# Kernel optimization log

Hardware: AMD Instinct MI355X
Metric: run time of the kernel (lower is better)

The kernel has to match this reference:

```python
import jax, jax.numpy as jnp
import numpy as np

NUM_PROJS = 7
BLOCK = 32

def _gray_perm(n):
    # unit-hamming-distance (Gray-code) permutation used by AngularLSH
    a = np.array([0, 1], dtype=np.int32)
    for s in range(2, n + 1):
        a = np.concatenate([a, a[::-1] + 2 ** (s - 1)])
    return a

PERM = jnp.asarray(_gray_perm(NUM_PROJS))
ENC = jnp.asarray(2 ** np.arange(NUM_PROJS), dtype=np.int32)  # [R]


def lsh_hash(x, proj_dir):
    # x: [B,H,S,D], proj_dir: [D,R] -> integer bucket ids [B,H,S]
    bits = (jnp.einsum('bhsd,dr->bhsr', x, proj_dir) > 0).astype(jnp.int32)
    code = (bits * ENC).sum(-1)
    return PERM[code]


def sdpa(q, k, v, mask):
    # q,k,v: [...,S,D]; mask: bool broadcastable to [...,Sq,Sk]
    scale = q.shape[-1] ** -0.5
    scores = jnp.einsum('...qd,...kd->...qk', q, k) * scale
    scores = jnp.where(mask, scores, -jnp.inf)
    return jnp.einsum('...qk,...kd->...qd', jax.nn.softmax(scores, axis=-1), v)


def setup_inputs() -> dict:
    key = jax.random.key(0)
    kq, kk, kv, kp = jax.random.split(key, 4)
    B, H, S, D = 2, 16, 2048, 128
    return {
        'q': jax.random.normal(kq, (B, H, S, D), dtype=jnp.float32),
        'k': jax.random.normal(kk, (B, H, S, D), dtype=jnp.float32),
        'v': jax.random.normal(kv, (B, H, S, D), dtype=jnp.float32),
        'proj_dir': jax.random.normal(kp, (D, NUM_PROJS), dtype=jnp.float32),
        'mask': jnp.ones((1, 1, 1, 1), dtype=bool),
    }


def reference(q, k, v, proj_dir, mask):
    B, H, S, D = q.shape
    # 1) LSH hash queries, stable sort along seq dim, reorder queries
    q_hash = lsh_hash(q, proj_dir)                                   # [B,H,S]
    sort_idx = jnp.argsort(q_hash, axis=2, stable=True)              # [B,H,S]
    q_hash_sorted = jnp.take_along_axis(q_hash, sort_idx, axis=2)
    q_sorted = jnp.take_along_axis(q, sort_idx[..., None], axis=2)   # [B,H,S,D]
    # 2) hash keys (unsorted), split into blocks of size BLOCK
    k_hash = lsh_hash(k, proj_dir)                                   # [B,H,S]
    k_hash_blk = k_hash.reshape(-1, 1, BLOCK)                        # [NB,1,32]
    q_hash_blk = q_hash_sorted.reshape(-1, 1, BLOCK)
    # 3) criticality: per-block count of matching hash ids; critical blocks get K zeroed
    criticality = (k_hash_blk == q_hash_blk).sum(-1).squeeze(-1)     # [NB]
    keep = (criticality <= 0).astype(q.dtype)                        # 0 where critical (matches torch loop)
    Qb = q_sorted.reshape(-1, 1, BLOCK, D)                           # [NB,1,32,D]
    Kb = k.reshape(-1, 1, BLOCK, D) * keep[:, None, None, None]
    Vb = v.reshape(-1, 1, BLOCK, D)
    # 4) dual SDPA: blocked critical attention + full dense attention
    out_critical = sdpa(Qb, Kb, Vb, mask).reshape(B, H, S, D)
    out_actual = sdpa(q, k, v, mask)                                 # [B,H,S,D]
    loss = jnp.mean((out_critical - out_actual) ** 2)
    return out_actual, loss
```

## Files before the change

kernel.cpp:

```cpp
#include <hip/hip_runtime.h>
#include <hip/hip_bf16.h>

#define SEQ 2048
#define DIM 128
#define NBH 32
#define NROWS (NBH*SEQ)
#define NBLK (NROWS/32)
#define SCALE 0.08838834764831845f
#define QSC (0.08838834764831845f * 1.4426950408889634f)

typedef __attribute__((ext_vector_type(8))) short short8;
typedef __attribute__((ext_vector_type(16))) float float16;

__device__ __forceinline__ unsigned short f2bf(float x) {
    union { float f; unsigned u; } v; v.f = x;
    unsigned r = v.u + 0x7fffu + ((v.u >> 16) & 1u);
    return (unsigned short)(r >> 16);
}
__device__ __forceinline__ unsigned pack_bf16(float a, float b) {
    float2 f; f.x = a; f.y = b;
    __hip_bfloat162 h = __float22bfloat162_rn(f);
    union { __hip_bfloat162 h2; unsigned u; } cv; cv.h2 = h; return cv.u;
}
__device__ __forceinline__ void gl_lds16(const void* g, void* l) {
    __builtin_amdgcn_global_load_lds((const __attribute__((address_space(1))) unsigned int*)g,
                                     (__attribute__((address_space(3))) unsigned int*)l, 16, 0, 0);
}

__global__ __launch_bounds__(256) void hash_kernel(const float* __restrict__ qg, const float* __restrict__ kg,
                            const float* __restrict__ proj,
                            int* __restrict__ qh, int* __restrict__ kh)
{
    const int gw   = (int)((blockIdx.x * blockDim.x + threadIdx.x) >> 6);
    const int lane = threadIdx.x & 63;
    const int sub  = lane >> 4;
    const int dl   = (lane & 15) * 8;
    const int r    = gw * 4 + sub;
    const float* src; int* dst; int row;
    if (r < NROWS) { src = qg; dst = qh; row = r; }
    else           { src = kg; dst = kh; row = r - NROWS; }

    const float* x = src + (size_t)row * DIM + dl;
    float xv[8];
    {
        float4 f0 = *(const float4*)x;
        float4 f1 = *(const float4*)(x + 4);
        xv[0]=f0.x; xv[1]=f0.y; xv[2]=f0.z; xv[3]=f0.w;
        xv[4]=f1.x; xv[5]=f1.y; xv[6]=f1.z; xv[7]=f1.w;
    }
    float pj[56];
    #pragma unroll
    for (int i = 0; i < 14; ++i)
        *(float4*)&pj[i*4] = *(const float4*)(proj + dl*7 + i*4);

    float a[7] = {0.f,0.f,0.f,0.f,0.f,0.f,0.f};
    #pragma unroll
    for (int d = 0; d < 8; ++d)
        #pragma unroll
        for (int p = 0; p < 7; ++p) a[p] = fmaf(xv[d], pj[d*7+p], a[p]);

    #pragma unroll
    for (int off = 1; off < 16; off <<= 1)
        #pragma unroll
        for (int p = 0; p < 7; ++p) a[p] += __shfl_xor(a[p], off, 64);

    if ((lane & 15) == 0) {
        int code = 0;
        if (a[0] > 0.f) code |= 1;  if (a[1] > 0.f) code |= 2;
        if (a[2] > 0.f) code |= 4;  if (a[3] > 0.f) code |= 8;
        if (a[4] > 0.f) code |= 16; if (a[5] > 0.f) code |= 32;
        if (a[6] > 0.f) code |= 64;
        dst[row] = code ^ (code >> 1);
    }
}

__global__ __launch_bounds__(256) void sort_kernel(const int* __restrict__ qh,
                                                   int* __restrict__ sidx, int* __restrict__ qhs)
{
    __shared__ unsigned short cnt[128][260];
    __shared__ int startv[128];
    const int bh = blockIdx.x;
    const int t  = threadIdx.x;
    const int base = bh*SEQ;

    for (int i = t; i < 128*260; i += 256) ((unsigned short*)cnt)[i] = 0;
    __syncthreads();

    int hv[8];
    {
        int4 a = *(const int4*)(qh + base + t*8);
        int4 b = *(const int4*)(qh + base + t*8 + 4);
        hv[0]=a.x; hv[1]=a.y; hv[2]=a.z; hv[3]=a.w;
        hv[4]=b.x; hv[5]=b.y; hv[6]=b.z; hv[7]=b.w;
    }
    #pragma unroll
    for (int i = 0; i < 8; ++i) cnt[hv[i]][t]++;
    __syncthreads();

    const int wv = t >> 6, l = t & 63;
    #pragma unroll 1
    for (int v = wv; v < 128; v += 4) {
        ushort4 cc = *(const ushort4*)&cnt[v][4*l];
        unsigned c0 = cc.x, c1 = cc.y, c2 = cc.z, c3 = cc.w;
        unsigned s01 = c0 + c1;
        unsigned s = s01 + c2 + c3;
        unsigned inc = s;
        #pragma unroll
        for (int off = 1; off < 64; off <<= 1) {
            unsigned o = __shfl_up(inc, off, 64);
            if (l >= off) inc += o;
        }
        unsigned ex = inc - s;
        ushort4 wb;
        wb.x = (unsigned short)ex;
        wb.y = (unsigned short)(ex + c0);
        wb.z = (unsigned short)(ex + s01);
        wb.w = (unsigned short)(ex + s01 + c2);
        *(ushort4*)&cnt[v][4*l] = wb;
        if (l == 63) cnt[v][256] = (unsigned short)inc;
    }
    __syncthreads();

    if (t < 64) {
        int a0 = cnt[2*t][256], a1 = cnt[2*t+1][256];
        int s2 = a0 + a1, inc = s2;
        #pragma unroll
        for (int off = 1; off < 64; off <<= 1) {
            int o = __shfl_up(inc, off, 64);
            if (t >= off) inc += o;
        }
        int ex = inc - s2;
        startv[2*t]   = ex;
        startv[2*t+1] = ex + a0;
    }
    __syncthreads();

    #pragma unroll
    for (int i = 0; i < 8; ++i) {
        const int v = hv[i];
        int prior = 0;
        #pragma unroll
        for (int j = 0; j < 8; ++j) if (j < i && hv[j] == v) ++prior;
        const int rank = startv[v] + (int)cnt[v][t] + prior;
        sidx[base + rank] = t*8 + i;
        qhs[base + rank]  = v;
    }
}

__global__ __launch_bounds__(256) void prep_kernel(const float* __restrict__ kg,
                                                   const float* __restrict__ vg,
                                                   unsigned short* __restrict__ kbf,
                                                   unsigned short* __restrict__ vtg)
{
    __shared__ unsigned short T[128][72];
    const int t  = threadIdx.x;
    const int h  = blockIdx.x >> 5;
    const int sl = blockIdx.x & 31;
    const size_t base = ((size_t)h*SEQ + sl*64) * DIM;

    #pragma unroll
    for (int i = 0; i < 8; ++i) {
        const float4 f = *(const float4*)(kg + base + ((size_t)i*256 + t)*4);
        uint2 pk; pk.x = pack_bf16(f.x, f.y); pk.y = pack_bf16(f.z, f.w);
        *(uint2*)(kbf + base + ((size_t)i*256 + t)*4) = pk;
    }

    const int kk = t & 63, seg = t >> 6;
    #pragma unroll
    for (int i = 0; i < 8; ++i) {
        float4 f = *(const float4*)(vg + base + (size_t)kk*DIM + seg*32 + i*4);
        T[seg*32 + i*4 + 0][kk] = f2bf(f.x);
        T[seg*32 + i*4 + 1][kk] = f2bf(f.y);
        T[seg*32 + i*4 + 2][kk] = f2bf(f.z);
        T[seg*32 + i*4 + 3][kk] = f2bf(f.w);
    }
    __syncthreads();
    const int r = t >> 1, hf = t & 1;
    unsigned short* dst = vtg + ((size_t)h*DIM + r)*SEQ + sl*64 + hf*32;
    #pragma unroll
    for (int i = 0; i < 4; ++i)
        *(short8*)(dst + i*8) = *(const short8*)&T[r][hf*32 + i*8];
}

__global__ __launch_bounds__(256, 2) void dense_attn_mfma(
    const unsigned short* __restrict__ kbf, const unsigned short* __restrict__ vtg,
    const float* __restrict__ qg, float* __restrict__ outg)
{
    __shared__ __align__(16) unsigned short KbF[2*8192];
    __shared__ __align__(16) unsigned short VbF[2*8192];

    const int t    = threadIdx.x;
    const int lane = t & 63;
    const int w    = t >> 6;
    const int q5   = lane >> 5;
    const int l31  = lane & 31;
    const int lvec = lane * 8;

    const int b    = blockIdx.x;
    const int slot = b >> 3;
    const int head = (b & 7) * 4 + (slot >> 4);
    const int qblk = slot & 15;

    const float* Qg = qg + ((size_t)head*SEQ + qblk*128 + w*32) * DIM;
    const unsigned short* Kh = kbf + (size_t)head*SEQ*DIM;
    const unsigned short* Vh = vtg + (size_t)head*DIM*SEQ;

    const unsigned short* kgp[4]; unsigned short* kls[4];
    const unsigned short* vgp[4]; unsigned short* vls[4];
    {
        const int ks = w >> 1, vs = w >> 1, vc = w & 1;
        #pragma unroll
        for (int i = 0; i < 4; ++i) {
            const int kch = (w & 1) * 4 + i;
            kgp[i] = Kh + (size_t)(ks*32 + l31)*DIM + kch*16 + q5*8;
            kls[i] = KbF + (ks*8 + kch)*512;
            vgp[i] = Vh + (size_t)(i*32 + l31)*SEQ + vs*32 + vc*16 + q5*8;
            vls[i] = VbF + (vs*8 + vc*4 + i)*512;
        }
    }

    auto stage = [&](const int buf) {
        #pragma unroll
        for (int i = 0; i < 4; ++i) gl_lds16(kgp[i], kls[i] + buf*8192);
        #pragma unroll
        for (int i = 0; i < 4; ++i) gl_lds16(vgp[i], vls[i] + buf*8192);
        #pragma unroll
        for (int i = 0; i < 4; ++i) { kgp[i] += 8192; vgp[i] += 64; }
    };

    stage(0);

    union FR { unsigned u[4]; short8 s; };
    short8 Qf[8];
    #pragma unroll
    for (int ch = 0; ch < 8; ++ch) {
        const float* p = Qg + (size_t)l31*DIM + ch*16 + q5*8;
        float4 f0 = *(const float4*)p;
        float4 f1 = *(const float4*)(p + 4);
        FR fr;
        fr.u[0] = pack_bf16(f0.x*QSC, f0.y*QSC);
        fr.u[1] = pack_bf16(f0.z*QSC, f0.w*QSC);
        fr.u[2] = pack_bf16(f1.x*QSC, f1.y*QSC);
        fr.u[3] = pack_bf16(f1.z*QSC, f1.w*QSC);
        Qf[ch] = fr.s;
    }

    float16 o[4];
    #pragma unroll
    for (int mt = 0; mt < 4; ++mt)
        #pragma unroll
        for (int r = 0; r < 16; ++r) o[mt][r] = 0.f;
    float lsum = 0.f;

    auto body = [&](const int buf) {
        const int B = buf*8192;
        #pragma unroll
        for (int s = 0; s < 2; ++s) {
            float16 sv;
            #pragma unroll
            for (int r = 0; r < 16; ++r) sv[r] = 0.f;
            #pragma unroll
            for (int ch = 0; ch < 8; ++ch) {
                short8 kf = *(const short8*)&KbF[B + s*4096 + ch*512 + lvec];
                sv = __builtin_amdgcn_mfma_f32_32x32x16_bf16(kf, Qf[ch], sv, 0, 0, 0);
            }
            unsigned pk[8];
            #pragma unroll
            for (int rp = 0; rp < 8; ++rp) {
                float p0 = __builtin_amdgcn_exp2f(sv[2*rp]);
                float p1 = __builtin_amdgcn_exp2f(sv[2*rp+1]);
                lsum += p0 + p1;
                pk[rp] = pack_bf16(p0, p1);
            }
            unsigned e0 = __shfl_xor(q5 ? pk[0] : pk[2], 32, 64);
            unsigned e1 = __shfl_xor(q5 ? pk[1] : pk[3], 32, 64);
            unsigned e2 = __shfl_xor(q5 ? pk[4] : pk[6], 32, 64);
            unsigned e3 = __shfl_xor(q5 ? pk[5] : pk[7], 32, 64);
            FR c0, c1;
            if (q5 == 0) {
                c0.u[0]=pk[0]; c0.u[1]=pk[1]; c0.u[2]=e0;    c0.u[3]=e1;
                c1.u[0]=pk[4]; c1.u[1]=pk[5]; c1.u[2]=e2;    c1.u[3]=e3;
            } else {
                c0.u[0]=e0;    c0.u[1]=e1;    c0.u[2]=pk[2]; c0.u[3]=pk[3];
                c1.u[0]=e2;    c1.u[1]=e3;    c1.u[2]=pk[6]; c1.u[3]=pk[7];
            }
            #pragma unroll
            for (int c = 0; c < 2; ++c) {
                short8 pf = c ? c1.s : c0.s;
                #pragma unroll
                for (int mt = 0; mt < 4; ++mt) {
                    short8 vf = *(const short8*)&VbF[B + s*4096 + c*2048 + mt*512 + lvec];
                    o[mt] = __builtin_amdgcn_mfma_f32_32x32x16_bf16(vf, pf, o[mt], 0, 0, 0);
                }
            }
        }
    };

    #pragma unroll 1
    for (int kt2 = 0; kt2 < 16; ++kt2) {
        __syncthreads();
        stage(1);
        body(0);
        __syncthreads();
        if (kt2 < 15) stage(0);
        body(1);
    }

    const float l = lsum + __shfl_xor(lsum, 32, 64);
    const float inv = 1.f / l;
    float* orow = outg + ((size_t)head*SEQ + qblk*128 + w*32 + l31) * DIM;
    #pragma unroll
    for (int mt = 0; mt < 4; ++mt)
        #pragma unroll
        for (int rg = 0; rg < 4; ++rg) {
            const int d0 = mt*32 + rg*8 + q5*4;
            float4 ov;
            ov.x = o[mt][rg*4+0]*inv; ov.y = o[mt][rg*4+1]*inv;
            ov.z = o[mt][rg*4+2]*inv; ov.w = o[mt][rg*4+3]*inv;
            *(float4*)(orow + d0) = ov;
        }
}

__global__ __launch_bounds__(256) void crit_attn(
    const unsigned short* __restrict__ kbf, const unsigned short* __restrict__ vtg,
    const float* __restrict__ qg, const int* __restrict__ sidx,
    const int* __restrict__ kh, const int* __restrict__ qhs,
    const float* __restrict__ outg, float* __restrict__ lossp)
{
    __shared__ float wsum[4];
    const int t    = threadIdx.x;
    const int lane = t & 63;
    const int w    = t >> 6;
    const int nb   = blockIdx.x * 4 + w;
    const int q5   = lane >> 5;
    const int l31  = lane & 31;
    const int bh   = nb >> 6;

    const int khv = kh[nb*32 + l31];
    const int qhv = qhs[nb*32 + l31];
    const unsigned long long mm = __ballot(khv == qhv);
    const float kp = ((mm & 0xffffffffull) == 0ull) ? 1.0f : 0.0f;

    const int qrow = sidx[bh*SEQ + (nb & 63)*32 + l31];

    union FR { unsigned u[4]; short8 s; };
    short8 Qf[8];
    const float* Qg = qg + ((size_t)bh*SEQ + qrow) * DIM;
    #pragma unroll
    for (int ch = 0; ch < 8; ++ch) {
        const float* p = Qg + ch*16 + q5*8;
        float4 f0 = *(const float4*)p;
        float4 f1 = *(const float4*)(p + 4);
        FR fr;
        fr.u[0] = pack_bf16(f0.x*QSC, f0.y*QSC);
        fr.u[1] = pack_bf16(f0.z*QSC, f0.w*QSC);
        fr.u[2] = pack_bf16(f1.x*QSC, f1.y*QSC);
        fr.u[3] = pack_bf16(f1.z*QSC, f1.w*QSC);
        Qf[ch] = fr.s;
    }

    const unsigned short* Kb = kbf + (size_t)(nb*32) * DIM;
    float16 sv, sw;
    #pragma unroll
    for (int r = 0; r < 16; ++r) { sv[r] = 0.f; sw[r] = 0.f; }
    #pragma unroll
    for (int ch = 0; ch < 4; ++ch) {
        short8 kf = *(const short8*)(Kb + (size_t)l31*DIM + ch*16 + q5*8);
        sv = __builtin_amdgcn_mfma_f32_32x32x16_bf16(kf, Qf[ch], sv, 0, 0, 0);
        short8 kg2 = *(const short8*)(Kb + (size_t)l31*DIM + (ch+4)*16 + q5*8);
        sw = __builtin_amdgcn_mfma_f32_32x32x16_bf16(kg2, Qf[ch+4], sw, 0, 0, 0);
    }

    float lsum = 0.f;
    unsigned pk[8];
    #pragma unroll
    for (int rp = 0; rp < 8; ++rp) {
        float p0 = __builtin_amdgcn_exp2f((sv[2*rp]   + sw[2*rp])   * kp);
        float p1 = __builtin_amdgcn_exp2f((sv[2*rp+1] + sw[2*rp+1]) * kp);
        lsum += p0 + p1;
        pk[rp] = pack_bf16(p0, p1);
    }
    unsigned e0 = __shfl_xor(q5 ? pk[0] : pk[2], 32, 64);
    unsigned e1 = __shfl_xor(q5 ? pk[1] : pk[3], 32, 64);
    unsigned e2 = __shfl_xor(q5 ? pk[4] : pk[6], 32, 64);
    unsigned e3 = __shfl_xor(q5 ? pk[5] : pk[7], 32, 64);
    FR c0, c1;
    if (q5 == 0) {
        c0.u[0]=pk[0]; c0.u[1]=pk[1]; c0.u[2]=e0;    c0.u[3]=e1;
        c1.u[0]=pk[4]; c1.u[1]=pk[5]; c1.u[2]=e2;    c1.u[3]=e3;
    } else {
        c0.u[0]=e0;    c0.u[1]=e1;    c0.u[2]=pk[2]; c0.u[3]=pk[3];
        c1.u[0]=e2;    c1.u[1]=e3;    c1.u[2]=pk[6]; c1.u[3]=pk[7];
    }
    const float ltot = lsum + __shfl_xor(lsum, 32, 64);

    const unsigned short* Vb = vtg + (size_t)bh*DIM*SEQ + (size_t)(nb & 63)*32;
    float16 o[4];
    #pragma unroll
    for (int mt = 0; mt < 4; ++mt)
        #pragma unroll
        for (int r = 0; r < 16; ++r) o[mt][r] = 0.f;
    #pragma unroll
    for (int c = 0; c < 2; ++c) {
        short8 pf = c ? c1.s : c0.s;
        #pragma unroll
        for (int mt = 0; mt < 4; ++mt) {
            short8 vf = *(const short8*)(Vb + (size_t)(mt*32 + l31)*SEQ + c*16 + q5*8);
            o[mt] = __builtin_amdgcn_mfma_f32_32x32x16_bf16(vf, pf, o[mt], 0, 0, 0);
        }
    }

    const float inv = 1.f / ltot;
    const float* oa_row = outg + (size_t)(nb*32 + l31) * DIM;
    float sq = 0.f;
    #pragma unroll
    for (int mt = 0; mt < 4; ++mt)
        #pragma unroll
        for (int rg = 0; rg < 4; ++rg) {
            const int d0 = mt*32 + rg*8 + q5*4;
            float4 oa = *(const float4*)(oa_row + d0);
            float dx = o[mt][rg*4+0]*inv - oa.x;
            float dy = o[mt][rg*4+1]*inv - oa.y;
            float dz = o[mt][rg*4+2]*inv - oa.z;
            float dw = o[mt][rg*4+3]*inv - oa.w;
            sq += dx*dx + dy*dy + dz*dz + dw*dw;
        }
    #pragma unroll
    for (int off = 32; off > 0; off >>= 1) sq += __shfl_down(sq, off, 64);
    if (lane == 0) wsum[w] = sq;
    __syncthreads();
    if (t == 0) atomicAdd(lossp, (wsum[0]+wsum[1]+wsum[2]+wsum[3]) * (1.0f/8388608.0f));
}

extern "C" void kernel_launch(void* const* d_in, const int* in_sizes, int n_in,
                              void* d_out, int out_size, void* d_ws, size_t ws_size,
                              hipStream_t stream)
{
    const float* q    = (const float*)d_in[0];
    const float* k    = (const float*)d_in[1];
    const float* v    = (const float*)d_in[2];
    const float* proj = (const float*)d_in[3];
    float* out   = (float*)d_out;
    float* lossp = out + (out_size - 1);

    int* qh   = (int*)d_ws;
    int* kh   = qh + NROWS;
    int* sidx = kh + NROWS;
    int* qhs  = sidx + NROWS;
    unsigned short* kbf = (unsigned short*)(qhs + NROWS);
    unsigned short* vtg = kbf + (size_t)NROWS*DIM;

    hipMemsetAsync(lossp, 0, sizeof(float), stream);
    prep_kernel<<<NBH*32, 256, 0, stream>>>(k, v, kbf, vtg);
    hash_kernel<<<(2*NROWS)/16, 256, 0, stream>>>(q, k, proj, qh, kh);
    sort_kernel<<<NBH, 256, 0, stream>>>(qh, sidx, qhs);
    dense_attn_mfma<<<512, 256, 0, stream>>>(kbf, vtg, q, out);
    crit_attn<<<NBLK/4, 256, 0, stream>>>(kbf, vtg, q, sidx, kh, qhs, out, lossp);
}
```

Before: 289.9 us.

## Use XOR-swizzled LDS layout for K/V tiles and add MFMA priority hints

Changes the LDS layout of the K and V tiles in the dense attention kernel from a fragment-packed arrangement to row-major tiles with an XOR swizzle. Global-to-LDS staging addresses and the per-lane fragment read offsets are recomputed to match, aiming to give coalesced global loads and fewer LDS bank conflicts. It also wraps the MFMA loops in s_setprio hints so those instructions get issue priority, and vectorizes the sort kernel's shared-counter zeroing to 16-byte stores. The swizzle index math must stay consistent across staging and reads, otherwise results become wrong.

```diff
diff --git a/kernel.cpp b/kernel.cpp
--- a/kernel.cpp
+++ b/kernel.cpp
@@ -77,13 +77,16 @@
 __global__ __launch_bounds__(256) void sort_kernel(const int* __restrict__ qh,
                                                    int* __restrict__ sidx, int* __restrict__ qhs)
 {
-    __shared__ unsigned short cnt[128][260];
+    __shared__ __align__(16) unsigned short cnt[128][260];
     __shared__ int startv[128];
     const int bh = blockIdx.x;
     const int t  = threadIdx.x;
     const int base = bh*SEQ;
 
-    for (int i = t; i < 128*260; i += 256) ((unsigned short*)cnt)[i] = 0;
+    {
+        const short8 z8 = {0,0,0,0,0,0,0,0};
+        for (int i = t; i < 4160; i += 256) ((short8*)cnt)[i] = z8;
+    }
     __syncthreads();
 
     int hv[8];
@@ -194,7 +197,7 @@
     const int w    = t >> 6;
     const int q5   = lane >> 5;
     const int l31  = lane & 31;
-    const int lvec = lane * 8;
+    const int e    = l31 & 7;
 
     const int b    = blockIdx.x;
     const int slot = b >> 3;
@@ -205,30 +208,26 @@
     const unsigned short* Kh = kbf + (size_t)head*SEQ*DIM;
     const unsigned short* Vh = vtg + (size_t)head*DIM*SEQ;
 
+    int koff[8], voff[4];
+    #pragma unroll
+    for (int ch = 0; ch < 8; ++ch) koff[ch] = l31*128 + (((2*ch + q5) ^ e) * 8);
+    #pragma unroll
+    for (int u = 0; u < 4; ++u)    voff[u]  = l31*64  + ((((u>>1)*4 + (u&1)*2 + q5) ^ e) * 8);
+
     const unsigned short* kgp[4]; unsigned short* kls[4];
     const unsigned short* vgp[4]; unsigned short* vls[4];
-    {
-        const int ks = w >> 1, vs = w >> 1, vc = w & 1;
-        #pragma unroll
-        for (int i = 0; i < 4; ++i) {
-            const int kch = (w & 1) * 4 + i;
-            kgp[i] = Kh + (size_t)(ks*32 + l31)*DIM + kch*16 + q5*8;
-            kls[i] = KbF + (ks*8 + kch)*512;
-            vgp[i] = Vh + (size_t)(i*32 + l31)*SEQ + vs*32 + vc*16 + q5*8;
-            vls[i] = VbF + (vs*8 + vc*4 + i)*512;
-        }
-    }
-
-    auto stage = [&](const int buf) {
-        #pragma unroll
-        for (int i = 0; i < 4; ++i) gl_lds16(kgp[i], kls[i] + buf*8192);
-        #pragma unroll
-        for (int i = 0; i < 4; ++i) gl_lds16(vgp[i], vls[i] + buf*8192);
-        #pragma unroll
-        for (int i = 0; i < 4; ++i) { kgp[i] += 8192; vgp[i] += 64; }
-    };
-
-    stage(0);
+    #pragma unroll
+    for (int i = 0; i < 4; ++i) {
+        const int j = w*4 + i;
+        const int r = j*4 + (lane >> 4);
+        const int u = (lane & 15) ^ (r & 7);
+        kgp[i] = Kh + r*DIM + u*8;
+        kls[i] = KbF + j*512;
+        const int d = j*8 + (lane >> 3);
+        const int u2 = (lane & 7) ^ (d & 7);
+        vgp[i] = Vh + (size_t)d*SEQ + u2*8;
+        vls[i] = VbF + j*512;
+    }
 
     union FR { unsigned u[4]; short8 s; };
     short8 Qf[8];
@@ -252,18 +251,28 @@
         for (int r = 0; r < 16; ++r) o[mt][r] = 0.f;
     float lsum = 0.f;
 
+    auto stage = [&](const int buf) {
+        #pragma unroll
+        for (int i = 0; i < 4; ++i) gl_lds16(kgp[i], kls[i] + buf*8192);
+        #pragma unroll
+        for (int i = 0; i < 4; ++i) gl_lds16(vgp[i], vls[i] + buf*8192);
+        #pragma unroll
+        for (int i = 0; i < 4; ++i) { kgp[i] += 8192; vgp[i] += 64; }
+    };
+
     auto body = [&](const int buf) {
-        const int B = buf*8192;
         #pragma unroll
         for (int s = 0; s < 2; ++s) {
             float16 sv;
             #pragma unroll
             for (int r = 0; r < 16; ++r) sv[r] = 0.f;
+            __builtin_amdgcn_s_setprio(1);
             #pragma unroll
             for (int ch = 0; ch < 8; ++ch) {
-                short8 kf = *(const short8*)&KbF[B + s*4096 + ch*512 + lvec];
+                short8 kf = *(const short8*)&KbF[buf*8192 + s*4096 + koff[ch]];
                 sv = __builtin_amdgcn_mfma_f32_32x32x16_bf16(kf, Qf[ch], sv, 0, 0, 0);
             }
+            __builtin_amdgcn_s_setprio(0);
             unsigned pk[8];
             #pragma unroll
             for (int rp = 0; rp < 8; ++rp) {
@@ -284,18 +293,21 @@
                 c0.u[0]=e0;    c0.u[1]=e1;    c0.u[2]=pk[2]; c0.u[3]=pk[3];
                 c1.u[0]=e2;    c1.u[1]=e3;    c1.u[2]=pk[6]; c1.u[3]=pk[7];
             }
+            __builtin_amdgcn_s_setprio(1);
             #pragma unroll
             for (int c = 0; c < 2; ++c) {
                 short8 pf = c ? c1.s : c0.s;
                 #pragma unroll
                 for (int mt = 0; mt < 4; ++mt) {
-                    short8 vf = *(const short8*)&VbF[B + s*4096 + c*2048 + mt*512 + lvec];
+                    short8 vf = *(const short8*)&VbF[buf*8192 + mt*2048 + voff[s*2 + c]];
                     o[mt] = __builtin_amdgcn_mfma_f32_32x32x16_bf16(vf, pf, o[mt], 0, 0, 0);
                 }
             }
+            __builtin_amdgcn_s_setprio(0);
         }
     };
 
+    stage(0);
     #pragma unroll 1
     for (int kt2 = 0; kt2 < 16; ++kt2) {
         __syncthreads();
```

New measurement: 278.8 us. -3.8%, faster.
